# Kernel tuning notes

Measured on AMD Instinct MI355X. Metric: run time of the kernel, lower is better.

The kernel has to match this reference:

```python
import jax, jax.numpy as jnp
import numpy as np


def _sobel_filters():
    # fil is the 3x3 smoothing kernel [[1,2,1],[2,4,2],[1,2,1]]
    fil = np.array([[1, 2, 1], [2, 4, 2], [1, 2, 1]], dtype=np.float32)
    fx = np.zeros((3, 3, 3), dtype=np.float32)
    fx[0, :, :] = fil
    fx[2, :, :] = -fil
    fy = np.zeros((3, 3, 3), dtype=np.float32)
    fy[:, 0, :] = fil
    fy[:, 2, :] = -fil
    fz = np.zeros((3, 3, 3), dtype=np.float32)
    fz[:, :, 0] = fil
    fz[:, :, 2] = -fil
    # Stack the three fixed (non-learned) filters as 3 output channels: [O=3, I=1, 3,3,3]
    return jnp.asarray(np.stack([fx, fy, fz])[:, None])


_FILT = _sobel_filters()
_DN = ('NCDHW', 'OIDHW', 'NCDHW')


def _grad3d(v):
    # v: [N,1,D,H,W] -> [N,3,D,H,W], padding=1 == SAME for 3x3x3 stride 1
    return jax.lax.conv_general_dilated(
        v, _FILT.astype(v.dtype), window_strides=(1, 1, 1),
        padding='SAME', dimension_numbers=_DN)


def setup_inputs() -> dict:
    key = jax.random.key(0)
    k1, k2 = jax.random.split(key)
    shape = (2, 1, 160, 192, 224)
    x = jax.random.normal(k1, shape, dtype=jnp.float32)
    y = jax.random.normal(k2, shape, dtype=jnp.float32)
    return {"x": x, "y": y}


def reference(x, y):
    gx = _grad3d(x)  # [N,3,D,H,W]
    gy = _grad3d(y)
    d2 = (gx - gy) ** 2
    # sum over the 3 directions of the per-direction MSE
    return jnp.sum(jnp.mean(d2, axis=(0, 2, 3, 4)))
```

## Files before the change

kernel.cpp:

```cpp
#include <hip/hip_runtime.h>
#include <stdint.h>


#define N_  2
#define D_  160
#define H_  192
#define W_  224
#define PS  (H_ * W_)

#define TD  10
#define TH  8
constexpr int SROWS = TH + 2;
constexpr int ROWF  = 224;
constexpr float SCALE = 1.0f / ((float)N_ * D_ * H_ * W_);

#define DMA16(gp, lp) __builtin_amdgcn_global_load_lds(                        \
    (const __attribute__((address_space(1))) void*)(gp),                       \
    (__attribute__((address_space(3))) void*)(lp), 16, 0, 0)

__global__ __launch_bounds__(256, 3)
void grad_loss_kernel(const float* __restrict__ x, const float* __restrict__ y,
                      float* __restrict__ out) {
    __shared__ float sbuf[3][SROWS][2][ROWF];
    __shared__ float wsum[4];

    const int tid  = threadIdx.x;
    const int lane = tid & 63;
    const int wv   = tid >> 6;

    const int h0 = blockIdx.y * TH;
    const int nchunks = D_ / TD;
    const int nb = blockIdx.z / nchunks;
    const int d0 = (blockIdx.z % nchunks) * TD;

    const float* vbx = x + (size_t)nb * ((size_t)D_ * PS);
    const float* vby = y + (size_t)nb * ((size_t)D_ * PS);

    int sl[5], sa[5], srw[5];
    const float* sb[5];
    #pragma unroll
    for (int k = 0; k < 5; ++k) {
        int item = 5 * wv + k;
        sl[k] = item >> 1;
        sa[k] = item & 1;
        int ghc = min(max(h0 - 1 + sl[k], 0), H_ - 1);
        srw[k] = ghc * W_;
        sb[k]  = sa[k] ? vby : vbx;
    }
    const int lo4 = lane * 4;

    auto stage = [&](int p, int bsel) {
        int pc = min(max(p, 0), D_ - 1);
        size_t poff = (size_t)pc * PS;
        if (lane < 56) {
            #pragma unroll
            for (int k = 0; k < 5; ++k)
                DMA16(sb[k] + poff + srw[k] + lo4, &sbuf[bsel][sl[k]][sa[k]][0]);
        }
    };

    const bool wact = lane < 56;
    float rmask[4];
    #pragma unroll
    for (int r = 0; r < 4; ++r) {
        int gh = h0 - 1 + 2 * wv + r;
        rmask[r] = (((unsigned)gh < (unsigned)H_) && wact) ? 1.f : 0.f;
    }
    const int lrd = (lane < 56 ? lane : 55) * 4;

    float4 A0[2], A1[2], A2[2], B0[2], B1[2], B2[2];
    const float4 z4 = make_float4(0.f, 0.f, 0.f, 0.f);
    #pragma unroll
    for (int j = 0; j < 2; ++j) { A0[j]=A1[j]=A2[j]=B0[j]=B1[j]=B2[j]=z4; }
    float acc = 0.f;

    stage(d0 - 1, 0);
    stage(d0,     1);

    for (int it = 0; it < TD + 2; ++it) {
        asm volatile("s_waitcnt vmcnt(5)\n\ts_barrier" ::: "memory");

        stage(d0 + 1 + it, (it + 2) % 3);

        const int q = d0 - 1 + it;
        const float pm = (q >= 0 && q < D_) ? 1.f : 0.f;
        const int bsel = it % 3;

        float4 sw[4], gw[4];
        #pragma unroll
        for (int r = 0; r < 4; ++r) {
            const int l = 2 * wv + r;
            const float4 xr = *(const float4*)&sbuf[bsel][l][0][lrd];
            const float4 yr = *(const float4*)&sbuf[bsel][l][1][lrd];
            const float m = rmask[r] * pm;
            float4 v = make_float4((xr.x - yr.x) * m, (xr.y - yr.y) * m,
                                   (xr.z - yr.z) * m, (xr.w - yr.w) * m);
            float Lm = __shfl_up(v.w, 1, 64);
            float Rp = __shfl_down(v.x, 1, 64);
            if (lane == 0) Lm = 0.f;
            sw[r] = make_float4(Lm + 2.f * v.x + v.y,
                                v.x + 2.f * v.y + v.z,
                                v.y + 2.f * v.z + v.w,
                                v.z + 2.f * v.w + Rp);
            gw[r] = make_float4(Lm - v.y, v.x - v.z, v.y - v.w, v.z - Rp);
        }
        float4 n0[2], n1[2], n2[2];
        #pragma unroll
        for (int j = 0; j < 2; ++j) {
            n0[j] = make_float4(sw[j].x + 2.f * sw[j+1].x + sw[j+2].x,
                                sw[j].y + 2.f * sw[j+1].y + sw[j+2].y,
                                sw[j].z + 2.f * sw[j+1].z + sw[j+2].z,
                                sw[j].w + 2.f * sw[j+1].w + sw[j+2].w);
            n1[j] = make_float4(sw[j].x - sw[j+2].x, sw[j].y - sw[j+2].y,
                                sw[j].z - sw[j+2].z, sw[j].w - sw[j+2].w);
            n2[j] = make_float4(gw[j].x + 2.f * gw[j+1].x + gw[j+2].x,
                                gw[j].y + 2.f * gw[j+1].y + gw[j+2].y,
                                gw[j].z + 2.f * gw[j+1].z + gw[j+2].z,
                                gw[j].w + 2.f * gw[j+1].w + gw[j+2].w);
        }

        if (it >= 2 && wact) {
            #pragma unroll
            for (int j = 0; j < 2; ++j) {
                float4 gx = make_float4(A0[j].x - n0[j].x, A0[j].y - n0[j].y,
                                        A0[j].z - n0[j].z, A0[j].w - n0[j].w);
                float4 gy = make_float4(A1[j].x + 2.f * B1[j].x + n1[j].x,
                                        A1[j].y + 2.f * B1[j].y + n1[j].y,
                                        A1[j].z + 2.f * B1[j].z + n1[j].z,
                                        A1[j].w + 2.f * B1[j].w + n1[j].w);
                float4 gz = make_float4(A2[j].x + 2.f * B2[j].x + n2[j].x,
                                        A2[j].y + 2.f * B2[j].y + n2[j].y,
                                        A2[j].z + 2.f * B2[j].z + n2[j].z,
                                        A2[j].w + 2.f * B2[j].w + n2[j].w);
                acc = fmaf(gx.x, gx.x, acc); acc = fmaf(gx.y, gx.y, acc);
                acc = fmaf(gx.z, gx.z, acc); acc = fmaf(gx.w, gx.w, acc);
                acc = fmaf(gy.x, gy.x, acc); acc = fmaf(gy.y, gy.y, acc);
                acc = fmaf(gy.z, gy.z, acc); acc = fmaf(gy.w, gy.w, acc);
                acc = fmaf(gz.x, gz.x, acc); acc = fmaf(gz.y, gz.y, acc);
                acc = fmaf(gz.z, gz.z, acc); acc = fmaf(gz.w, gz.w, acc);
            }
        }

        #pragma unroll
        for (int j = 0; j < 2; ++j) {
            A0[j] = B0[j]; A1[j] = B1[j]; A2[j] = B2[j];
            B0[j] = n0[j]; B1[j] = n1[j]; B2[j] = n2[j];
        }
    }

    asm volatile("s_waitcnt vmcnt(0)" ::: "memory");

    #pragma unroll
    for (int off = 32; off > 0; off >>= 1)
        acc += __shfl_xor(acc, off, 64);
    if (lane == 0) wsum[wv] = acc;
    __syncthreads();
    if (tid == 0) {
        float s = (wsum[0] + wsum[1]) + (wsum[2] + wsum[3]);
        atomicAdd(out, s * SCALE);
    }
}

extern "C" void kernel_launch(void* const* d_in, const int* in_sizes, int n_in,
                              void* d_out, int out_size, void* d_ws, size_t ws_size,
                              hipStream_t stream) {
    const float* x = (const float*)d_in[0];
    const float* y = (const float*)d_in[1];
    float* out = (float*)d_out;

    hipMemsetAsync(out, 0, sizeof(float), stream);

    dim3 block(256);
    dim3 grid(1,
              H_ / TH,
              N_ * (D_ / TD));
    grad_loss_kernel<<<grid, block, 0, stream>>>(x, y, out);
}
```

Measured before the change: 144.3 us.

## Replace LDS DMA staging with direct per-wave register prefetch of rows

Removes the shared-memory triple buffer filled by global_load_lds along with its per-iteration waitcnt and barrier. Each wave instead loads its own four halo rows of x and y directly into registers, prefetching the next depth plane while computing the current one. This removes LDS usage and block-level synchronisation but duplicates overlapping halo-row loads across waves and relies on L2 to absorb them. The stencil accumulation is also regrouped to use FMAs incrementally.

Result: faster. 134.3 us (-6.9%).

```diff
diff --git a/kernel.cpp b/kernel.cpp
--- a/kernel.cpp
+++ b/kernel.cpp
@@ -10,63 +10,59 @@
 
 #define TD  10
 #define TH  8
-constexpr int SROWS = TH + 2;
-constexpr int ROWF  = 224;
 constexpr float SCALE = 1.0f / ((float)N_ * D_ * H_ * W_);
 
-#define DMA16(gp, lp) __builtin_amdgcn_global_load_lds(                        \
-    (const __attribute__((address_space(1))) void*)(gp),                       \
-    (__attribute__((address_space(3))) void*)(lp), 16, 0, 0)
+__device__ __forceinline__ float4 f4add(float4 a, float4 b) {
+    return make_float4(a.x + b.x, a.y + b.y, a.z + b.z, a.w + b.w);
+}
+__device__ __forceinline__ float4 f4sub(float4 a, float4 b) {
+    return make_float4(a.x - b.x, a.y - b.y, a.z - b.z, a.w - b.w);
+}
+__device__ __forceinline__ float4 f4fma(float k, float4 a, float4 b) {
+    return make_float4(fmaf(k, a.x, b.x), fmaf(k, a.y, b.y),
+                       fmaf(k, a.z, b.z), fmaf(k, a.w, b.w));
+}
 
 __global__ __launch_bounds__(256, 3)
 void grad_loss_kernel(const float* __restrict__ x, const float* __restrict__ y,
                       float* __restrict__ out) {
-    __shared__ float sbuf[3][SROWS][2][ROWF];
     __shared__ float wsum[4];
 
     const int tid  = threadIdx.x;
     const int lane = tid & 63;
     const int wv   = tid >> 6;
 
-    const int h0 = blockIdx.y * TH;
     const int nchunks = D_ / TD;
     const int nb = blockIdx.z / nchunks;
     const int d0 = (blockIdx.z % nchunks) * TD;
+    const int h0w = blockIdx.y * TH + 2 * wv;
 
     const float* vbx = x + (size_t)nb * ((size_t)D_ * PS);
     const float* vby = y + (size_t)nb * ((size_t)D_ * PS);
 
-    int sl[5], sa[5], srw[5];
-    const float* sb[5];
-    #pragma unroll
-    for (int k = 0; k < 5; ++k) {
-        int item = 5 * wv + k;
-        sl[k] = item >> 1;
-        sa[k] = item & 1;
-        int ghc = min(max(h0 - 1 + sl[k], 0), H_ - 1);
-        srw[k] = ghc * W_;
-        sb[k]  = sa[k] ? vby : vbx;
-    }
-    const int lo4 = lane * 4;
-
-    auto stage = [&](int p, int bsel) {
-        int pc = min(max(p, 0), D_ - 1);
-        size_t poff = (size_t)pc * PS;
-        if (lane < 56) {
-            #pragma unroll
-            for (int k = 0; k < 5; ++k)
-                DMA16(sb[k] + poff + srw[k] + lo4, &sbuf[bsel][sl[k]][sa[k]][0]);
-        }
-    };
-
     const bool wact = lane < 56;
+    const int lo4c = (lane < 56 ? lane : 55) * 4;
+    int off[4];
     float rmask[4];
     #pragma unroll
     for (int r = 0; r < 4; ++r) {
-        int gh = h0 - 1 + 2 * wv + r;
+        int gh  = h0w - 1 + r;
+        int ghc = min(max(gh, 0), H_ - 1);
+        off[r]   = ghc * W_ + lo4c;
         rmask[r] = (((unsigned)gh < (unsigned)H_) && wact) ? 1.f : 0.f;
     }
-    const int lrd = (lane < 56 ? lane : 55) * 4;
+
+    float4 XR[8];
+    auto loadp = [&](int p) {
+        int pc = min(max(p, 0), D_ - 1);
+        const float* bx = vbx + (size_t)pc * PS;
+        const float* by = vby + (size_t)pc * PS;
+        #pragma unroll
+        for (int r = 0; r < 4; ++r) {
+            XR[2 * r]     = *(const float4*)(bx + off[r]);
+            XR[2 * r + 1] = *(const float4*)(by + off[r]);
+        }
+    };
 
     float4 A0[2], A1[2], A2[2], B0[2], B1[2], B2[2];
     const float4 z4 = make_float4(0.f, 0.f, 0.f, 0.f);
@@ -74,64 +70,57 @@
     for (int j = 0; j < 2; ++j) { A0[j]=A1[j]=A2[j]=B0[j]=B1[j]=B2[j]=z4; }
     float acc = 0.f;
 
-    stage(d0 - 1, 0);
-    stage(d0,     1);
+    loadp(d0 - 1);
 
     for (int it = 0; it < TD + 2; ++it) {
-        asm volatile("s_waitcnt vmcnt(5)\n\ts_barrier" ::: "memory");
-
-        stage(d0 + 1 + it, (it + 2) % 3);
-
         const int q = d0 - 1 + it;
         const float pm = (q >= 0 && q < D_) ? 1.f : 0.f;
-        const int bsel = it % 3;
 
-        float4 sw[4], gw[4];
+        float4 v[4];
         #pragma unroll
         for (int r = 0; r < 4; ++r) {
-            const int l = 2 * wv + r;
-            const float4 xr = *(const float4*)&sbuf[bsel][l][0][lrd];
-            const float4 yr = *(const float4*)&sbuf[bsel][l][1][lrd];
             const float m = rmask[r] * pm;
-            float4 v = make_float4((xr.x - yr.x) * m, (xr.y - yr.y) * m,
-                                   (xr.z - yr.z) * m, (xr.w - yr.w) * m);
-            float Lm = __shfl_up(v.w, 1, 64);
-            float Rp = __shfl_down(v.x, 1, 64);
-            if (lane == 0) Lm = 0.f;
-            sw[r] = make_float4(Lm + 2.f * v.x + v.y,
-                                v.x + 2.f * v.y + v.z,
-                                v.y + 2.f * v.z + v.w,
-                                v.z + 2.f * v.w + Rp);
-            gw[r] = make_float4(Lm - v.y, v.x - v.z, v.y - v.w, v.z - Rp);
+            v[r] = make_float4((XR[2*r].x - XR[2*r+1].x) * m,
+                               (XR[2*r].y - XR[2*r+1].y) * m,
+                               (XR[2*r].z - XR[2*r+1].z) * m,
+                               (XR[2*r].w - XR[2*r+1].w) * m);
         }
+
+        if (it <= TD) loadp(d0 + it);
+
         float4 n0[2], n1[2], n2[2];
         #pragma unroll
-        for (int j = 0; j < 2; ++j) {
-            n0[j] = make_float4(sw[j].x + 2.f * sw[j+1].x + sw[j+2].x,
-                                sw[j].y + 2.f * sw[j+1].y + sw[j+2].y,
-                                sw[j].z + 2.f * sw[j+1].z + sw[j+2].z,
-                                sw[j].w + 2.f * sw[j+1].w + sw[j+2].w);
-            n1[j] = make_float4(sw[j].x - sw[j+2].x, sw[j].y - sw[j+2].y,
-                                sw[j].z - sw[j+2].z, sw[j].w - sw[j+2].w);
-            n2[j] = make_float4(gw[j].x + 2.f * gw[j+1].x + gw[j+2].x,
-                                gw[j].y + 2.f * gw[j+1].y + gw[j+2].y,
-                                gw[j].z + 2.f * gw[j+1].z + gw[j+2].z,
-                                gw[j].w + 2.f * gw[j+1].w + gw[j+2].w);
+        for (int r = 0; r < 4; ++r) {
+            const float4 vv = v[r];
+            float Lm = __shfl_up(vv.w, 1, 64);
+            float Rp = __shfl_down(vv.x, 1, 64);
+            if (lane == 0) Lm = 0.f;
+            const float4 s = make_float4(Lm + 2.f * vv.x + vv.y,
+                                         vv.x + 2.f * vv.y + vv.z,
+                                         vv.y + 2.f * vv.z + vv.w,
+                                         vv.z + 2.f * vv.w + Rp);
+            const float4 g = make_float4(Lm - vv.y, vv.x - vv.z,
+                                         vv.y - vv.w, vv.z - Rp);
+            if (r == 0) { n0[0] = s;                 n1[0] = s;
+                          n2[0] = g; }
+            if (r == 1) { n0[0] = f4fma(2.f, s, n0[0]);
+                          n2[0] = f4fma(2.f, g, n2[0]);
+                          n0[1] = s;                 n1[1] = s;
+                          n2[1] = g; }
+            if (r == 2) { n0[0] = f4add(n0[0], s);   n1[0] = f4sub(n1[0], s);
+                          n2[0] = f4add(n2[0], g);
+                          n0[1] = f4fma(2.f, s, n0[1]);
+                          n2[1] = f4fma(2.f, g, n2[1]); }
+            if (r == 3) { n0[1] = f4add(n0[1], s);   n1[1] = f4sub(n1[1], s);
+                          n2[1] = f4add(n2[1], g); }
         }
 
-        if (it >= 2 && wact) {
+        if (it >= 2) {
             #pragma unroll
             for (int j = 0; j < 2; ++j) {
-                float4 gx = make_float4(A0[j].x - n0[j].x, A0[j].y - n0[j].y,
-                                        A0[j].z - n0[j].z, A0[j].w - n0[j].w);
-                float4 gy = make_float4(A1[j].x + 2.f * B1[j].x + n1[j].x,
-                                        A1[j].y + 2.f * B1[j].y + n1[j].y,
-                                        A1[j].z + 2.f * B1[j].z + n1[j].z,
-                                        A1[j].w + 2.f * B1[j].w + n1[j].w);
-                float4 gz = make_float4(A2[j].x + 2.f * B2[j].x + n2[j].x,
-                                        A2[j].y + 2.f * B2[j].y + n2[j].y,
-                                        A2[j].z + 2.f * B2[j].z + n2[j].z,
-                                        A2[j].w + 2.f * B2[j].w + n2[j].w);
+                const float4 gx = f4sub(A0[j], n0[j]);
+                const float4 gy = f4add(f4fma(2.f, B1[j], A1[j]), n1[j]);
+                const float4 gz = f4add(f4fma(2.f, B2[j], A2[j]), n2[j]);
                 acc = fmaf(gx.x, gx.x, acc); acc = fmaf(gx.y, gx.y, acc);
                 acc = fmaf(gx.z, gx.z, acc); acc = fmaf(gx.w, gx.w, acc);
                 acc = fmaf(gy.x, gy.x, acc); acc = fmaf(gy.y, gy.y, acc);
@@ -148,11 +137,9 @@
         }
     }
 
-    asm volatile("s_waitcnt vmcnt(0)" ::: "memory");
-
     #pragma unroll
-    for (int off = 32; off > 0; off >>= 1)
-        acc += __shfl_xor(acc, off, 64);
+    for (int off_ = 32; off_ > 0; off_ >>= 1)
+        acc += __shfl_xor(acc, off_, 64);
     if (lane == 0) wsum[wv] = acc;
     __syncthreads();
     if (tid == 0) {
```
